# Optimization experiments

Measured on AMD Instinct MI355X. Metric: run time of the kernel, lower is better.

Reference implementation:

```python
import jax, jax.numpy as jnp
import numpy as np

N, E, D_IN, D_OUT = 50000, 800000, 128, 128
EPS = 1e-5


def setup_inputs() -> dict:
    key = jax.random.key(0)
    ks = jax.random.split(key, 6)
    x = jax.random.normal(ks[0], (N, D_IN), dtype=jnp.float32)
    edge_index = jax.random.randint(ks[1], (2, E), 0, N, dtype=jnp.int64)
    # dropout mask with keep-prob 0.5, inverted-dropout scaling
    dropout_mask = (jax.random.uniform(ks[2], (N, D_IN)) > 0.5).astype(jnp.float32) * 2.0
    ln_weight = jnp.ones((D_IN,), jnp.float32)
    ln_bias = jnp.zeros((D_IN,), jnp.float32)
    w_l = jax.random.normal(ks[3], (D_IN, D_OUT), jnp.float32) / np.float32(np.sqrt(D_IN))
    b_l = jnp.zeros((D_OUT,), jnp.float32)
    w_r = jax.random.normal(ks[4], (D_IN, D_OUT), jnp.float32) / np.float32(np.sqrt(D_IN))
    return dict(x=x, edge_index=edge_index, dropout_mask=dropout_mask,
                ln_weight=ln_weight, ln_bias=ln_bias, w_l=w_l, b_l=b_l, w_r=w_r)


def reference(x, edge_index, dropout_mask, ln_weight, ln_bias, w_l, b_l, w_r):
    # PyG graph-mode LayerNorm (batch=None): normalize over all nodes & channels
    xc = x - jnp.mean(x)
    h = xc / (jnp.std(xc) + EPS) * ln_weight + ln_bias
    h = jax.nn.relu(h) * dropout_mask  # training path with dropout mask
    # SAGEConv (mean aggregation): aggregate source features into destinations
    src, dst = edge_index[0], edge_index[1]
    msg = h[src]  # [E, D_IN] gather
    agg = jax.ops.segment_sum(msg, dst, num_segments=N)  # [N, D_IN] scatter-add
    deg = jax.ops.segment_sum(jnp.ones((E,), h.dtype), dst, num_segments=N)
    agg = agg / jnp.maximum(deg, 1.0)[:, None]
    # out = lin_l(mean_aggr) + lin_r(x_root)
    return agg @ w_l + b_l + h @ w_r
```

## Files before the change

### kernel.cpp

```cpp
#include <hip/hip_runtime.h>
#include <math.h>

#define N_NODES 50000
#define N_EDGES 800000
#define D 128
#define EPS 1e-5f

#define WS_STATS_OFF   0
#define WS_CUR_OFF     16
#define WS_DEG_OFF     64
#define WS_OFFS_OFF    200192
#define WS_BUCKET_OFF  400448
#define WS_W16T_OFF    3600448
#define WS_AGG_OFF     3731520
#define WS_H_OFF       16531520
#define WS_ZERO_BYTES  200192

#define RED_BLOCKS 1024
#define DEG_BLOCKS ((N_EDGES + 255) / 256)
#define H_BLOCKS   2048
#define FILL_BLOCKS DEG_BLOCKS

typedef __attribute__((ext_vector_type(8))) short short8v;
typedef __attribute__((ext_vector_type(4))) float f32x4;

static __device__ inline unsigned short f2bf(float f) {
    unsigned u = __float_as_uint(f);
    return (unsigned short)((u + 0x7FFFu + ((u >> 16) & 1u)) >> 16);
}
static __device__ inline float bf2f(unsigned short s) {
    return __uint_as_float(((unsigned)s) << 16);
}

__global__ __launch_bounds__(256) void k_pre(const float* __restrict__ x,
                                             const int* __restrict__ ei,
                                             double* __restrict__ stats,
                                             int* __restrict__ deg,
                                             int total4) {
    __shared__ float bs[4], bss[4];
    if (blockIdx.x < RED_BLOCKS) {
        int tid = blockIdx.x * 256 + threadIdx.x;
        int stride = RED_BLOCKS * 256;
        float s = 0.f, ss = 0.f;
        for (int i = tid; i < total4; i += stride) {
            float4 v = ((const float4*)x)[i];
            s  += v.x + v.y + v.z + v.w;
            ss += v.x*v.x + v.y*v.y + v.z*v.z + v.w*v.w;
        }
        for (int off = 32; off; off >>= 1) {
            s  += __shfl_down(s, off);
            ss += __shfl_down(ss, off);
        }
        int lane = threadIdx.x & 63, wid = threadIdx.x >> 6;
        if (lane == 0) { bs[wid] = s; bss[wid] = ss; }
        __syncthreads();
        if (threadIdx.x == 0) {
            float t = 0.f, tt = 0.f;
            for (int w = 0; w < 4; ++w) { t += bs[w]; tt += bss[w]; }
            atomicAdd(stats, (double)t);
            atomicAdd(stats + 1, (double)tt);
        }
    } else {
        int e = (blockIdx.x - RED_BLOCKS) * 256 + threadIdx.x;
        if (e < N_EDGES) atomicAdd(deg + ei[N_EDGES + e], 1);
    }
}

__global__ __launch_bounds__(256) void k_wprep(const float* __restrict__ w_l,
                                               const float* __restrict__ w_r,
                                               unsigned short* __restrict__ w16t) {
    int t = blockIdx.x * 256 + threadIdx.x;
    int p = t >> 12;
    int o = (t >> 5) & 127;
    int k4 = t & 31;
    const float* w = p ? w_r : w_l;
    ushort4 hi, lo;
    float v0 = w[(k4 * 4 + 0) * D + o];
    float v1 = w[(k4 * 4 + 1) * D + o];
    float v2 = w[(k4 * 4 + 2) * D + o];
    float v3 = w[(k4 * 4 + 3) * D + o];
    hi.x = f2bf(v0); lo.x = f2bf(v0 - bf2f(hi.x));
    hi.y = f2bf(v1); lo.y = f2bf(v1 - bf2f(hi.y));
    hi.z = f2bf(v2); lo.z = f2bf(v2 - bf2f(hi.z));
    hi.w = f2bf(v3); lo.w = f2bf(v3 - bf2f(hi.w));
    *(ushort4*)(w16t + p * 32768 + o * D + k4 * 4) = hi;
    *(ushort4*)(w16t + p * 32768 + 16384 + o * D + k4 * 4) = lo;
}

__global__ __launch_bounds__(256) void k_offs(const int* __restrict__ deg,
                                              int* __restrict__ offs,
                                              int* __restrict__ cursor) {
    __shared__ int sc[256];
    __shared__ int sbase;
    int t = threadIdx.x;
    int n = blockIdx.x * 256 + t;
    int d = (n < N_NODES) ? deg[n] : 0;
    sc[t] = d;
    __syncthreads();
    for (int off = 1; off < 256; off <<= 1) {
        int u = (t >= off) ? sc[t - off] : 0;
        __syncthreads();
        sc[t] += u;
        __syncthreads();
    }
    int incl = sc[t];
    if (t == 255) sbase = atomicAdd(cursor, incl);
    __syncthreads();
    if (n < N_NODES) offs[n] = sbase + (incl - d);
}

__global__ __launch_bounds__(256) void k_hfill(const float* __restrict__ x,
                                               const float* __restrict__ mask,
                                               const float* __restrict__ lnw,
                                               const float* __restrict__ lnb,
                                               const double* __restrict__ stats,
                                               const int* __restrict__ ei,
                                               int* __restrict__ offs,
                                               int* __restrict__ bucket,
                                               unsigned short* __restrict__ h16,
                                               int total4) {
    if (blockIdx.x < H_BLOCKS) {
        double M = (double)N_NODES * (double)D;
        double mean_d = stats[0] / M;
        double var = stats[1] / M - mean_d * mean_d;
        if (var < 0.0) var = 0.0;
        float mean = (float)mean_d;
        float rstd = (float)(1.0 / (sqrt(var) + (double)EPS));
        int tid = blockIdx.x * 256 + threadIdx.x;
        int stride = H_BLOCKS * 256;
        for (int i = tid; i < total4; i += stride) {
            float4 v = ((const float4*)x)[i];
            float4 m = ((const float4*)mask)[i];
            int c4 = i & (D / 4 - 1);
            float4 w = ((const float4*)lnw)[c4];
            float4 b = ((const float4*)lnb)[c4];
            float4 r;
            r.x = fmaxf((v.x - mean) * rstd * w.x + b.x, 0.f) * m.x;
            r.y = fmaxf((v.y - mean) * rstd * w.y + b.y, 0.f) * m.y;
            r.z = fmaxf((v.z - mean) * rstd * w.z + b.z, 0.f) * m.z;
            r.w = fmaxf((v.w - mean) * rstd * w.w + b.w, 0.f) * m.w;
            ushort4 o;
            o.x = f2bf(r.x); o.y = f2bf(r.y); o.z = f2bf(r.z); o.w = f2bf(r.w);
            ((ushort4*)h16)[i] = o;
        }
    } else {
        int e = (blockIdx.x - H_BLOCKS) * 256 + threadIdx.x;
        if (e < N_EDGES) {
            int dst = ei[N_EDGES + e];
            int p = atomicAdd(offs + dst, 1);
            bucket[p] = ei[e];
        }
    }
}

__global__ __launch_bounds__(256) void k_agg(const int* __restrict__ bucket,
                                             const int* __restrict__ offs,
                                             const int* __restrict__ deg,
                                             const unsigned short* __restrict__ h16,
                                             unsigned short* __restrict__ agg16) {
    int t = blockIdx.x * blockDim.x + threadIdx.x;
    int node = t >> 5;
    if (node >= N_NODES) return;
    int c = t & 31;
    int dg = deg[node];
    int end = offs[node];
    int start = end - dg;
    float4 acc = {0.f, 0.f, 0.f, 0.f};
    for (int j = start; j < end; ++j) {
        int src = bucket[j];
        uint2 u = *(const uint2*)(h16 + (long long)src * D + c * 4);
        acc.x += __uint_as_float(u.x << 16);
        acc.y += __uint_as_float(u.x & 0xFFFF0000u);
        acc.z += __uint_as_float(u.y << 16);
        acc.w += __uint_as_float(u.y & 0xFFFF0000u);
    }
    float inv = 1.0f / fmaxf((float)dg, 1.0f);
    ushort4 o;
    o.x = f2bf(acc.x * inv); o.y = f2bf(acc.y * inv);
    o.z = f2bf(acc.z * inv); o.w = f2bf(acc.w * inv);
    *(ushort4*)(agg16 + (long long)node * D + c * 4) = o;
}

__global__ __launch_bounds__(256) void k_mmf(const unsigned short* __restrict__ agg16,
                                             const unsigned short* __restrict__ h16,
                                             const unsigned short* __restrict__ w16t,
                                             const float* __restrict__ b_l,
                                             float* __restrict__ out) {
    int wid = (blockIdx.x << 2) | (threadIdx.x >> 6);
    int lane = threadIdx.x & 63;
    int nt = wid >> 3;
    int ot = wid & 7;
    int rc = lane & 15;
    int kg = lane >> 4;

    const unsigned short* pa = agg16 + ((long long)(nt * 16 + rc)) * D + kg * 8;
    const unsigned short* ph = h16   + ((long long)(nt * 16 + rc)) * D + kg * 8;
    const unsigned short* bl_hi = w16t + (ot * 16 + rc) * D + kg * 8;
    const unsigned short* bl_lo = bl_hi + 16384;
    const unsigned short* br_hi = bl_hi + 32768;
    const unsigned short* br_lo = bl_hi + 49152;

    f32x4 acc = {0.f, 0.f, 0.f, 0.f};
#pragma unroll
    for (int k0 = 0; k0 < 4; ++k0) {
        short8v a = *(const short8v*)(pa + k0 * 32);
        acc = __builtin_amdgcn_mfma_f32_16x16x32_bf16(a, *(const short8v*)(bl_hi + k0 * 32), acc, 0, 0, 0);
        acc = __builtin_amdgcn_mfma_f32_16x16x32_bf16(a, *(const short8v*)(bl_lo + k0 * 32), acc, 0, 0, 0);
    }
#pragma unroll
    for (int k0 = 0; k0 < 4; ++k0) {
        short8v a = *(const short8v*)(ph + k0 * 32);
        acc = __builtin_amdgcn_mfma_f32_16x16x32_bf16(a, *(const short8v*)(br_hi + k0 * 32), acc, 0, 0, 0);
        acc = __builtin_amdgcn_mfma_f32_16x16x32_bf16(a, *(const short8v*)(br_lo + k0 * 32), acc, 0, 0, 0);
    }

    float bias = b_l[ot * 16 + rc];
    float* op = out + ((long long)(nt * 16 + kg * 4)) * D + ot * 16 + rc;
#pragma unroll
    for (int r = 0; r < 4; ++r)
        op[(long long)r * D] = acc[r] + bias;
}

extern "C" void kernel_launch(void* const* d_in, const int* in_sizes, int n_in,
                              void* d_out, int out_size, void* d_ws, size_t ws_size,
                              hipStream_t stream) {
    const float* x    = (const float*)d_in[0];
    const int*   ei   = (const int*)d_in[1];
    const float* mask = (const float*)d_in[2];
    const float* lnw  = (const float*)d_in[3];
    const float* lnb  = (const float*)d_in[4];
    const float* w_l  = (const float*)d_in[5];
    const float* b_l  = (const float*)d_in[6];
    const float* w_r  = (const float*)d_in[7];
    float* out = (float*)d_out;

    char* ws = (char*)d_ws;
    double* stats = (double*)(ws + WS_STATS_OFF);
    int*    cursor= (int*)(ws + WS_CUR_OFF);
    int*    deg   = (int*)(ws + WS_DEG_OFF);
    int*    offs  = (int*)(ws + WS_OFFS_OFF);
    int*    bucket= (int*)(ws + WS_BUCKET_OFF);
    unsigned short* w16t  = (unsigned short*)(ws + WS_W16T_OFF);
    unsigned short* agg16 = (unsigned short*)(ws + WS_AGG_OFF);
    unsigned short* h16   = (unsigned short*)(ws + WS_H_OFF);

    hipMemsetAsync(d_ws, 0, WS_ZERO_BYTES, stream);

    int total4 = N_NODES * D / 4;
    k_pre<<<RED_BLOCKS + DEG_BLOCKS, 256, 0, stream>>>(x, ei, stats, deg, total4);
    k_wprep<<<32, 256, 0, stream>>>(w_l, w_r, w16t);
    k_offs<<<(N_NODES + 255) / 256, 256, 0, stream>>>(deg, offs, cursor);
    k_hfill<<<H_BLOCKS + FILL_BLOCKS, 256, 0, stream>>>(x, mask, lnw, lnb, stats,
                                                        ei, offs, bucket, h16, total4);
    int ablocks = (N_NODES * 32 + 255) / 256;
    k_agg<<<ablocks, 256, 0, stream>>>(bucket, offs, deg, h16, agg16);
    int mblocks = (N_NODES / 16) * 8 / 4;
    k_mmf<<<mblocks, 256, 0, stream>>>(agg16, h16, w16t, b_l, out);
}
```

Measured before the change: 333.5 us.

## Stage weights in swizzled LDS and compute full output rows per wave

```diff
diff --git a/kernel.cpp b/kernel.cpp
--- a/kernel.cpp
+++ b/kernel.cpp
@@ -20,6 +20,10 @@
 #define DEG_BLOCKS ((N_EDGES + 255) / 256)
 #define H_BLOCKS   2048
 #define FILL_BLOCKS DEG_BLOCKS
+
+#define MM_BLOCKS 256
+#define MM_SLOTS  (MM_BLOCKS * 8)
+#define MM_TILES  (N_NODES / 16)
 
 typedef __attribute__((ext_vector_type(8))) short short8v;
 typedef __attribute__((ext_vector_type(4))) float f32x4;
@@ -181,44 +185,78 @@
     *(ushort4*)(agg16 + (long long)node * D + c * 4) = o;
 }
 
-__global__ __launch_bounds__(256) void k_mmf(const unsigned short* __restrict__ agg16,
-                                             const unsigned short* __restrict__ h16,
-                                             const unsigned short* __restrict__ w16t,
-                                             const float* __restrict__ b_l,
-                                             float* __restrict__ out) {
-    int wid = (blockIdx.x << 2) | (threadIdx.x >> 6);
-    int lane = threadIdx.x & 63;
-    int nt = wid >> 3;
-    int ot = wid & 7;
+__global__ __launch_bounds__(512, 2) void k_mmf(const unsigned short* __restrict__ agg16,
+                                                const unsigned short* __restrict__ h16,
+                                                const unsigned short* __restrict__ w16t,
+                                                const float* __restrict__ b_l,
+                                                float* __restrict__ out) {
+    __shared__ uint4 lds4[4096];
+    unsigned char* ldsb = (unsigned char*)lds4;
+    int tid  = threadIdx.x;
+    int wave = tid >> 6;
+    int lane = tid & 63;
     int rc = lane & 15;
     int kg = lane >> 4;
-
-    const unsigned short* pa = agg16 + ((long long)(nt * 16 + rc)) * D + kg * 8;
-    const unsigned short* ph = h16   + ((long long)(nt * 16 + rc)) * D + kg * 8;
-    const unsigned short* bl_hi = w16t + (ot * 16 + rc) * D + kg * 8;
-    const unsigned short* bl_lo = bl_hi + 16384;
-    const unsigned short* br_hi = bl_hi + 32768;
-    const unsigned short* br_lo = bl_hi + 49152;
-
-    f32x4 acc = {0.f, 0.f, 0.f, 0.f};
-#pragma unroll
-    for (int k0 = 0; k0 < 4; ++k0) {
-        short8v a = *(const short8v*)(pa + k0 * 32);
-        acc = __builtin_amdgcn_mfma_f32_16x16x32_bf16(a, *(const short8v*)(bl_hi + k0 * 32), acc, 0, 0, 0);
-        acc = __builtin_amdgcn_mfma_f32_16x16x32_bf16(a, *(const short8v*)(bl_lo + k0 * 32), acc, 0, 0, 0);
-    }
-#pragma unroll
-    for (int k0 = 0; k0 < 4; ++k0) {
-        short8v a = *(const short8v*)(ph + k0 * 32);
-        acc = __builtin_amdgcn_mfma_f32_16x16x32_bf16(a, *(const short8v*)(br_hi + k0 * 32), acc, 0, 0, 0);
-        acc = __builtin_amdgcn_mfma_f32_16x16x32_bf16(a, *(const short8v*)(br_lo + k0 * 32), acc, 0, 0, 0);
-    }
-
-    float bias = b_l[ot * 16 + rc];
-    float* op = out + ((long long)(nt * 16 + kg * 4)) * D + ot * 16 + rc;
-#pragma unroll
-    for (int r = 0; r < 4; ++r)
-        op[(long long)r * D] = acc[r] + bias;
+    int slot = blockIdx.x * 8 + wave;
+    int nt0 = slot;
+    int nt1 = slot + MM_SLOTS;
+    bool has1 = (nt1 < MM_TILES);
+    int sx = (rc & 7) << 4;
+
+    f32x4 acc0[8], acc1[8];
+#pragma unroll
+    for (int ot = 0; ot < 8; ++ot) { acc0[ot] = {0.f,0.f,0.f,0.f}; acc1[ot] = {0.f,0.f,0.f,0.f}; }
+
+#pragma unroll
+    for (int phase = 0; phase < 2; ++phase) {
+        if (phase) __syncthreads();
+        {
+            const uint4* src = (const uint4*)(w16t + phase * 32768);
+#pragma unroll
+            for (int i = 0; i < 8; ++i) {
+                int idx = i * 512 + tid;
+                int byteoff = idx * 16;
+                int swz = byteoff ^ (((idx >> 4) & 7) << 4);
+                *(uint4*)(ldsb + swz) = src[idx];
+            }
+        }
+        __syncthreads();
+
+        const unsigned short* abase = phase ? h16 : agg16;
+        const unsigned short* pa0 = abase + (long long)(nt0 * 16 + rc) * D + kg * 8;
+        const unsigned short* pa1 = abase + (long long)((has1 ? nt1 : nt0) * 16 + rc) * D + kg * 8;
+
+#pragma unroll
+        for (int k0 = 0; k0 < 4; ++k0) {
+            short8v a0 = *(const short8v*)(pa0 + k0 * 32);
+            short8v a1 = *(const short8v*)(pa1 + k0 * 32);
+#pragma unroll
+            for (int ot = 0; ot < 8; ++ot) {
+                int bo = (ot * 16 + rc) * 256 + kg * 16 + k0 * 64;
+                short8v bhi = *(const short8v*)(ldsb + (bo ^ sx));
+                short8v blo = *(const short8v*)(ldsb + ((bo + 32768) ^ sx));
+                acc0[ot] = __builtin_amdgcn_mfma_f32_16x16x32_bf16(a0, bhi, acc0[ot], 0, 0, 0);
+                acc0[ot] = __builtin_amdgcn_mfma_f32_16x16x32_bf16(a0, blo, acc0[ot], 0, 0, 0);
+                if (has1) {
+                    acc1[ot] = __builtin_amdgcn_mfma_f32_16x16x32_bf16(a1, bhi, acc1[ot], 0, 0, 0);
+                    acc1[ot] = __builtin_amdgcn_mfma_f32_16x16x32_bf16(a1, blo, acc1[ot], 0, 0, 0);
+                }
+            }
+        }
+    }
+
+#pragma unroll
+    for (int ot = 0; ot < 8; ++ot) {
+        float bias = b_l[ot * 16 + rc];
+        float* op0 = out + (long long)(nt0 * 16 + kg * 4) * D + ot * 16 + rc;
+#pragma unroll
+        for (int r = 0; r < 4; ++r) op0[(long long)r * D] = acc0[ot][r] + bias;
+        if (has1) {
+            float* op1 = out + (long long)(nt1 * 16 + kg * 4) * D + ot * 16 + rc;
+#pragma unroll
+            for (int r = 0; r < 4; ++r) op1[(long long)r * D] = acc1[ot][r] + bias;
+        }
+    }
 }
 
 extern "C" void kernel_launch(void* const* d_in, const int* in_sizes, int n_in,
@@ -254,6 +292,5 @@
                                                         ei, offs, bucket, h16, total4);
     int ablocks = (N_NODES * 32 + 255) / 256;
     k_agg<<<ablocks, 256, 0, stream>>>(bucket, offs, deg, h16, agg16);
-    int mblocks = (N_NODES / 16) * 8 / 4;
-    k_mmf<<<mblocks, 256, 0, stream>>>(agg16, h16, w16t, b_l, out);
-}
+    k_mmf<<<MM_BLOCKS, 512, 0, stream>>>(agg16, h16, w16t, b_l, out);
+}
```

Result: slower. 488.5 us (+46.5%).
